# Kernel tuning notes

Hardware: AMD Instinct MI355X
Metric: run time of the kernel (lower is better)

## Reference

```python
import jax, jax.numpy as jnp
import numpy as np

N_NODES = 10000
N_EDGES = 320000
IN_DIM = 256
OUT_DIM = 256
LN_EPS = 1e-5


def setup_inputs() -> dict:
    key = jax.random.key(0)
    ks = jax.random.split(key, 4)
    x = jax.random.normal(ks[0], (N_NODES, IN_DIM), dtype=jnp.float32)
    edge_index = jax.random.randint(ks[1], (2, N_EDGES), 0, N_NODES, dtype=jnp.int64)
    # Linear weights stored input-major so y = x @ W + b
    W_msg = jax.random.normal(ks[2], (2 * IN_DIM, OUT_DIM), dtype=jnp.float32) / np.sqrt(2 * IN_DIM)
    b_msg = jnp.zeros((OUT_DIM,), dtype=jnp.float32)
    W_upd = jax.random.normal(ks[3], (IN_DIM + OUT_DIM, OUT_DIM), dtype=jnp.float32) / np.sqrt(IN_DIM + OUT_DIM)
    b_upd = jnp.zeros((OUT_DIM,), dtype=jnp.float32)
    gamma = jnp.ones((OUT_DIM,), dtype=jnp.float32)
    beta = jnp.zeros((OUT_DIM,), dtype=jnp.float32)
    return {"x": x, "edge_index": edge_index, "W_msg": W_msg, "b_msg": b_msg,
            "W_upd": W_upd, "b_upd": b_upd, "gamma": gamma, "beta": beta}


def reference(x, edge_index, W_msg, b_msg, W_upd, b_upd, gamma, beta):
    row, col = edge_index[0], edge_index[1]
    # gather -> concat -> linear -> relu   [E, out_dim]
    msg_in = jnp.concatenate([x[row], x[col]], axis=-1)
    messages = jax.nn.relu(msg_in @ W_msg + b_msg)
    # scatter-add aggregate over destination nodes  [N, out_dim]
    aggregated = jax.ops.segment_sum(messages, col, num_segments=x.shape[0])
    # update: concat -> linear -> relu -> layernorm
    h = jax.nn.relu(jnp.concatenate([x, aggregated], axis=-1) @ W_upd + b_upd)
    mu = jnp.mean(h, axis=-1, keepdims=True)
    var = jnp.mean(jnp.square(h - mu), axis=-1, keepdims=True)
    return (h - mu) * jax.lax.rsqrt(var + LN_EPS) * gamma + beta
```

## Files before the change

### kernel.cpp

```cpp
#include <hip/hip_runtime.h>
#include <hip/hip_bf16.h>
#include <stdint.h>

#define NNODES 10000
#define NEDGES 320000
#define DIM    256
#define KTOT   512
#define LN_EPS 1e-5f
#define BCAP   96

typedef __attribute__((ext_vector_type(4))) float f32x4;
typedef __attribute__((ext_vector_type(8))) short bf16x8;

__device__ __forceinline__ ushort f2bf(float f) {
    union { float f; uint32_t u; } v; v.f = f;
    uint32_t r = v.u + 0x7fffu + ((v.u >> 16) & 1u);
    return (ushort)(r >> 16);
}
__device__ __forceinline__ float bf2f(ushort u) {
    union { float f; uint32_t u; } v; v.u = ((uint32_t)u) << 16;
    return v.f;
}

__global__ __launch_bounds__(256)
void prep_all(const float* __restrict__ x, const float* __restrict__ Wm,
              const float* __restrict__ Wu, ushort* __restrict__ xb,
              ushort* __restrict__ Wcat, ushort* __restrict__ Wua,
              int4* __restrict__ cntz) {
    int tid = blockIdx.x * 256 + threadIdx.x;
    if (tid < 2560) cntz[tid] = (int4){0, 0, 0, 0};
    if (tid < 640000) {
        float4 v = reinterpret_cast<const float4*>(x)[tid];
        ushort4 o;
        o.x = f2bf(v.x); o.y = f2bf(v.y); o.z = f2bf(v.z); o.w = f2bf(v.w);
        reinterpret_cast<ushort4*>(xb)[tid] = o;
    } else {
        int t = tid - 640000;
        if (t < 131072) {
            int kk  = t >> 14;
            int rem = t & 16383;
            int g   = rem >> 9;
            int kg  = (rem >> 7) & 3;
            int ml  = (rem >> 3) & 15;
            int j   = rem & 7;
            int k = kk * 32 + kg * 8 + j;
            int n = g * 16 + ml;
            float v = (n < 256) ? Wm[k * DIM + n] : Wm[(k + 256) * DIM + (n - 256)];
            Wcat[t] = f2bf(v);
        } else {
            int rem = t - 131072;
            int kk  = rem >> 13;
            int nt  = (rem >> 9) & 15;
            int kg  = (rem >> 7) & 3;
            int ml  = (rem >> 3) & 15;
            int j   = rem & 7;
            int k = kk * 32 + kg * 8 + j;
            int n = nt * 16 + ml;
            Wua[rem] = f2bf(Wu[k * DIM + n]);
        }
    }
}

__global__ __launch_bounds__(512)
void scatter_uv(const int* __restrict__ eidx, int* __restrict__ cnt,
                int* __restrict__ srow, const ushort* __restrict__ xb,
                const ushort* __restrict__ Wcat, const float* __restrict__ bmsg,
                ushort* __restrict__ Ub, float* __restrict__ Vf) {
    if (blockIdx.x < 1250) {
        int e = blockIdx.x * 256 + (threadIdx.x & 255);
        if (threadIdx.x < 256) {
            int d = eidx[NEDGES + e];
            int p = atomicAdd(&cnt[d], 1);
            if (p < BCAP) srow[d * BCAP + p] = eidx[e];
        }
        return;
    }
    const int wave = threadIdx.x >> 6;
    const int lane = threadIdx.x & 63;
    const int ml = lane & 15, kg = lane >> 4;
    const int wr = wave >> 2, wc = wave & 3;
    const int nb = (blockIdx.x - 1250) * 64;

    uint arow[2];
#pragma unroll
    for (int t = 0; t < 2; ++t) {
        int n = nb + wr * 32 + t * 16 + ml;
        arow[t] = (uint)(n < NNODES ? n : NNODES - 1) * DIM;
    }

    f32x4 acc[2][8];
#pragma unroll
    for (int t = 0; t < 2; ++t)
#pragma unroll
        for (int nt = 0; nt < 8; ++nt) acc[t][nt] = (f32x4){0.f, 0.f, 0.f, 0.f};

#pragma unroll
    for (int kk = 0; kk < 8; ++kk) {
        bf16x8 a0 = *reinterpret_cast<const bf16x8*>(xb + arow[0] + kk * 32 + kg * 8);
        bf16x8 a1 = *reinterpret_cast<const bf16x8*>(xb + arow[1] + kk * 32 + kg * 8);
#pragma unroll
        for (int nt = 0; nt < 8; ++nt) {
            bf16x8 b = *reinterpret_cast<const bf16x8*>(Wcat + kk * 16384 + (wc * 8 + nt) * 512 + lane * 8);
            acc[0][nt] = __builtin_amdgcn_mfma_f32_16x16x32_bf16(a0, b, acc[0][nt], 0, 0, 0);
            acc[1][nt] = __builtin_amdgcn_mfma_f32_16x16x32_bf16(a1, b, acc[1][nt], 0, 0, 0);
        }
    }

    if (wc < 2) {
#pragma unroll
        for (int t = 0; t < 2; ++t)
#pragma unroll
            for (int nt = 0; nt < 8; ++nt) {
                const int col = wc * 128 + nt * 16 + ml;
#pragma unroll
                for (int i = 0; i < 4; ++i) {
                    int node = nb + wr * 32 + t * 16 + kg * 4 + i;
                    if (node < NNODES) Ub[(size_t)node * 256 + col] = f2bf(acc[t][nt][i]);
                }
            }
    } else {
#pragma unroll
        for (int t = 0; t < 2; ++t)
#pragma unroll
            for (int nt = 0; nt < 8; ++nt) {
                const int col = (wc - 2) * 128 + nt * 16 + ml;
                const float bb = bmsg[col];
#pragma unroll
                for (int i = 0; i < 4; ++i) {
                    int node = nb + wr * 32 + t * 16 + kg * 4 + i;
                    if (node < NNODES) Vf[(size_t)node * 256 + col] = acc[t][nt][i] + bb;
                }
            }
    }
}

__global__ __launch_bounds__(256)
void edge_combine(const ushort* __restrict__ Ub, const float* __restrict__ Vf,
                  const int* __restrict__ srow, const int* __restrict__ cnt,
                  ushort* __restrict__ aggb) {
    const int wave = threadIdx.x >> 6, lane = threadIdx.x & 63;
    const int nb = blockIdx.x * 8;
    const int el = lane >> 5;
    const int cl = lane & 31;
    const int c0 = cl * 8;

#pragma unroll
    for (int nn = 0; nn < 2; ++nn) {
        const int d = nb + wave * 2 + nn;
        int deg = cnt[d]; deg = deg < BCAP ? deg : BCAP;
        const int beg = d * BCAP;
        const float4 va = *reinterpret_cast<const float4*>(&Vf[(size_t)d * 256 + c0]);
        const float4 vb = *reinterpret_cast<const float4*>(&Vf[(size_t)d * 256 + c0 + 4]);
        float s[8];
#pragma unroll
        for (int j = 0; j < 8; ++j) s[j] = 0.f;

#define ACC8(U) do { \
        s[0] += fmaxf(bf2f((ushort)(U)[0]) + va.x, 0.f); \
        s[1] += fmaxf(bf2f((ushort)(U)[1]) + va.y, 0.f); \
        s[2] += fmaxf(bf2f((ushort)(U)[2]) + va.z, 0.f); \
        s[3] += fmaxf(bf2f((ushort)(U)[3]) + va.w, 0.f); \
        s[4] += fmaxf(bf2f((ushort)(U)[4]) + vb.x, 0.f); \
        s[5] += fmaxf(bf2f((ushort)(U)[5]) + vb.y, 0.f); \
        s[6] += fmaxf(bf2f((ushort)(U)[6]) + vb.z, 0.f); \
        s[7] += fmaxf(bf2f((ushort)(U)[7]) + vb.w, 0.f); } while (0)

        int i = el;
        for (; i + 6 < deg; i += 8) {
            int r0 = srow[beg + i],     r1 = srow[beg + i + 2];
            int r2 = srow[beg + i + 4], r3 = srow[beg + i + 6];
            bf16x8 u0 = *reinterpret_cast<const bf16x8*>(&Ub[(size_t)r0 * 256 + c0]);
            bf16x8 u1 = *reinterpret_cast<const bf16x8*>(&Ub[(size_t)r1 * 256 + c0]);
            bf16x8 u2 = *reinterpret_cast<const bf16x8*>(&Ub[(size_t)r2 * 256 + c0]);
            bf16x8 u3 = *reinterpret_cast<const bf16x8*>(&Ub[(size_t)r3 * 256 + c0]);
            ACC8(u0); ACC8(u1); ACC8(u2); ACC8(u3);
        }
        for (; i < deg; i += 2) {
            int r = srow[beg + i];
            bf16x8 u = *reinterpret_cast<const bf16x8*>(&Ub[(size_t)r * 256 + c0]);
            ACC8(u);
        }
#undef ACC8
#pragma unroll
        for (int j = 0; j < 8; ++j) s[j] += __shfl_xor(s[j], 32);
        if (el == 0) {
            union { bf16x8 v; ushort h[8]; } o;
#pragma unroll
            for (int j = 0; j < 8; ++j) o.h[j] = f2bf(s[j]);
            *reinterpret_cast<bf16x8*>(&aggb[(size_t)d * 256 + c0]) = o.v;
        }
    }
}

__global__ __launch_bounds__(512)
void node_ln(const ushort* __restrict__ xb, const ushort* __restrict__ aggb,
             const ushort* __restrict__ Wua, const float* __restrict__ bupd,
             const float* __restrict__ gamma, const float* __restrict__ beta,
             float* __restrict__ out) {
    __shared__ float pS[64][4][2];

    const int wave = threadIdx.x >> 6;
    const int lane = threadIdx.x & 63;
    const int ml = lane & 15, kg = lane >> 4;
    const int wr = wave >> 2, wc = wave & 3;
    const int nb = blockIdx.x * 64;

    uint arow[2];
#pragma unroll
    for (int t = 0; t < 2; ++t) {
        int n = nb + wr * 32 + t * 16 + ml;
        arow[t] = (uint)(n < NNODES ? n : NNODES - 1) * DIM;
    }

    f32x4 acc[2][4];
#pragma unroll
    for (int t = 0; t < 2; ++t)
#pragma unroll
        for (int nt = 0; nt < 4; ++nt) acc[t][nt] = (f32x4){0.f, 0.f, 0.f, 0.f};

#pragma unroll
    for (int kk = 0; kk < 8; ++kk) {
        bf16x8 a0 = *reinterpret_cast<const bf16x8*>(xb + arow[0] + kk * 32 + kg * 8);
        bf16x8 a1 = *reinterpret_cast<const bf16x8*>(xb + arow[1] + kk * 32 + kg * 8);
#pragma unroll
        for (int nt = 0; nt < 4; ++nt) {
            bf16x8 b = *reinterpret_cast<const bf16x8*>(Wua + kk * 8192 + (wc * 4 + nt) * 512 + lane * 8);
            acc[0][nt] = __builtin_amdgcn_mfma_f32_16x16x32_bf16(a0, b, acc[0][nt], 0, 0, 0);
            acc[1][nt] = __builtin_amdgcn_mfma_f32_16x16x32_bf16(a1, b, acc[1][nt], 0, 0, 0);
        }
    }
#pragma unroll
    for (int kk = 0; kk < 8; ++kk) {
        bf16x8 a0 = *reinterpret_cast<const bf16x8*>(aggb + arow[0] + kk * 32 + kg * 8);
        bf16x8 a1 = *reinterpret_cast<const bf16x8*>(aggb + arow[1] + kk * 32 + kg * 8);
#pragma unroll
        for (int nt = 0; nt < 4; ++nt) {
            bf16x8 b = *reinterpret_cast<const bf16x8*>(Wua + 65536 + kk * 8192 + (wc * 4 + nt) * 512 + lane * 8);
            acc[0][nt] = __builtin_amdgcn_mfma_f32_16x16x32_bf16(a0, b, acc[0][nt], 0, 0, 0);
            acc[1][nt] = __builtin_amdgcn_mfma_f32_16x16x32_bf16(a1, b, acc[1][nt], 0, 0, 0);
        }
    }

    float sum[2][4], ssq[2][4];
#pragma unroll
    for (int t = 0; t < 2; ++t)
#pragma unroll
        for (int i = 0; i < 4; ++i) { sum[t][i] = 0.f; ssq[t][i] = 0.f; }
#pragma unroll
    for (int t = 0; t < 2; ++t)
#pragma unroll
        for (int nt = 0; nt < 4; ++nt) {
            const float bb = bupd[wc * 64 + nt * 16 + ml];
#pragma unroll
            for (int i = 0; i < 4; ++i) {
                float v = acc[t][nt][i] + bb;
                v = v > 0.f ? v : 0.f;
                acc[t][nt][i] = v;
                sum[t][i] += v;
                ssq[t][i] += v * v;
            }
        }
#pragma unroll
    for (int m = 1; m < 16; m <<= 1) {
#pragma unroll
        for (int t = 0; t < 2; ++t)
#pragma unroll
            for (int i = 0; i < 4; ++i) {
                sum[t][i] += __shfl_xor(sum[t][i], m);
                ssq[t][i] += __shfl_xor(ssq[t][i], m);
            }
    }
    if (ml == 0) {
#pragma unroll
        for (int t = 0; t < 2; ++t)
#pragma unroll
            for (int i = 0; i < 4; ++i) {
                int nl = wr * 32 + t * 16 + kg * 4 + i;
                pS[nl][wc][0] = sum[t][i];
                pS[nl][wc][1] = ssq[t][i];
            }
    }
    __syncthreads();

    float mu[2][4], rs[2][4];
#pragma unroll
    for (int t = 0; t < 2; ++t)
#pragma unroll
        for (int i = 0; i < 4; ++i) {
            int nl = wr * 32 + t * 16 + kg * 4 + i;
            float S = pS[nl][0][0] + pS[nl][1][0] + pS[nl][2][0] + pS[nl][3][0];
            float Q = pS[nl][0][1] + pS[nl][1][1] + pS[nl][2][1] + pS[nl][3][1];
            float m = S * (1.f / 256.f);
            float var = Q * (1.f / 256.f) - m * m;
            mu[t][i] = m;
            rs[t][i] = rsqrtf(var + LN_EPS);
        }
#pragma unroll
    for (int t = 0; t < 2; ++t)
#pragma unroll
        for (int nt = 0; nt < 4; ++nt) {
            const int cc = wc * 64 + nt * 16 + ml;
            const float g = gamma[cc], be = beta[cc];
#pragma unroll
            for (int i = 0; i < 4; ++i) {
                const int node = nb + wr * 32 + t * 16 + kg * 4 + i;
                if (node < NNODES)
                    out[(size_t)node * DIM + cc] = (acc[t][nt][i] - mu[t][i]) * rs[t][i] * g + be;
            }
        }
}

extern "C" void kernel_launch(void* const* d_in, const int* in_sizes, int n_in,
                              void* d_out, int out_size, void* d_ws, size_t ws_size,
                              hipStream_t stream) {
    const float* x    = (const float*)d_in[0];
    const int*   eidx = (const int*)  d_in[1];
    const float* Wm   = (const float*)d_in[2];
    const float* bm   = (const float*)d_in[3];
    const float* Wu   = (const float*)d_in[4];
    const float* bu   = (const float*)d_in[5];
    const float* gam  = (const float*)d_in[6];
    const float* bet  = (const float*)d_in[7];
    float* out = (float*)d_out;

    char* ws = (char*)d_ws;
    ushort* xb     = (ushort*)(ws);
    ushort* Ub     = (ushort*)(ws +  5120000);
    float*  Vf     = (float*) (ws + 10240000);
    ushort* aggb   = (ushort*)(ws + 20480000);
    ushort* Wcat   = (ushort*)(ws + 25600000);
    ushort* Wua    = (ushort*)(ws + 25862144);
    int*    cnt    = (int*)   (ws + 26124288);
    int*    srow   = (int*)   (ws + 26165248);

    prep_all<<<3524, 256, 0, stream>>>(x, Wm, Wu, xb, Wcat, Wua, (int4*)cnt);
    scatter_uv<<<1407, 512, 0, stream>>>(eidx, cnt, srow, xb, Wcat, bm, Ub, Vf);
    edge_combine<<<1250, 256, 0, stream>>>(Ub, Vf, srow, cnt, aggb);
    node_ln<<<157, 512, 0, stream>>>(xb, aggb, Wua, bu, gam, bet, out);
}
```

Before: 87.41 us.

## Batch edge scatter per thread, shrink srow to ushort, retile node GEMM blocks

```diff
diff --git a/kernel.cpp b/kernel.cpp
--- a/kernel.cpp
+++ b/kernel.cpp
@@ -61,82 +61,75 @@
     }
 }
 
-__global__ __launch_bounds__(512)
+__global__ __launch_bounds__(256)
 void scatter_uv(const int* __restrict__ eidx, int* __restrict__ cnt,
-                int* __restrict__ srow, const ushort* __restrict__ xb,
+                ushort* __restrict__ srow, const ushort* __restrict__ xb,
                 const ushort* __restrict__ Wcat, const float* __restrict__ bmsg,
                 ushort* __restrict__ Ub, float* __restrict__ Vf) {
-    if (blockIdx.x < 1250) {
-        int e = blockIdx.x * 256 + (threadIdx.x & 255);
-        if (threadIdx.x < 256) {
-            int d = eidx[NEDGES + e];
-            int p = atomicAdd(&cnt[d], 1);
-            if (p < BCAP) srow[d * BCAP + p] = eidx[e];
-        }
+    if (blockIdx.x < 320) {
+        const int t = blockIdx.x * 256 + threadIdx.x;
+        int d[4], r[4];
+#pragma unroll
+        for (int j = 0; j < 3; ++j) {
+            int e = t + j * 81920;
+            d[j] = eidx[NEDGES + e];
+            r[j] = eidx[e];
+        }
+        const bool ok3 = t < (NEDGES - 3 * 81920);
+        if (ok3) { d[3] = eidx[NEDGES + t + 245760]; r[3] = eidx[t + 245760]; }
+        int p[4];
+#pragma unroll
+        for (int j = 0; j < 3; ++j) p[j] = atomicAdd(&cnt[d[j]], 1);
+        if (ok3) p[3] = atomicAdd(&cnt[d[3]], 1);
+#pragma unroll
+        for (int j = 0; j < 3; ++j)
+            if (p[j] < BCAP) srow[d[j] * BCAP + p[j]] = (ushort)r[j];
+        if (ok3 && p[3] < BCAP) srow[d[3] * BCAP + p[3]] = (ushort)r[3];
         return;
     }
-    const int wave = threadIdx.x >> 6;
+    const int wq   = threadIdx.x >> 6;
     const int lane = threadIdx.x & 63;
     const int ml = lane & 15, kg = lane >> 4;
-    const int wr = wave >> 2, wc = wave & 3;
-    const int nb = (blockIdx.x - 1250) * 64;
-
-    uint arow[2];
-#pragma unroll
-    for (int t = 0; t < 2; ++t) {
-        int n = nb + wr * 32 + t * 16 + ml;
-        arow[t] = (uint)(n < NNODES ? n : NNODES - 1) * DIM;
-    }
-
-    f32x4 acc[2][8];
-#pragma unroll
-    for (int t = 0; t < 2; ++t)
-#pragma unroll
-        for (int nt = 0; nt < 8; ++nt) acc[t][nt] = (f32x4){0.f, 0.f, 0.f, 0.f};
+    const int nb = (blockIdx.x - 320) * 16;
+    const uint arow = (uint)(nb + ml) * DIM;
+
+    f32x4 acc[8];
+#pragma unroll
+    for (int nt = 0; nt < 8; ++nt) acc[nt] = (f32x4){0.f, 0.f, 0.f, 0.f};
 
 #pragma unroll
     for (int kk = 0; kk < 8; ++kk) {
-        bf16x8 a0 = *reinterpret_cast<const bf16x8*>(xb + arow[0] + kk * 32 + kg * 8);
-        bf16x8 a1 = *reinterpret_cast<const bf16x8*>(xb + arow[1] + kk * 32 + kg * 8);
+        bf16x8 a = *reinterpret_cast<const bf16x8*>(xb + arow + kk * 32 + kg * 8);
 #pragma unroll
         for (int nt = 0; nt < 8; ++nt) {
-            bf16x8 b = *reinterpret_cast<const bf16x8*>(Wcat + kk * 16384 + (wc * 8 + nt) * 512 + lane * 8);
-            acc[0][nt] = __builtin_amdgcn_mfma_f32_16x16x32_bf16(a0, b, acc[0][nt], 0, 0, 0);
-            acc[1][nt] = __builtin_amdgcn_mfma_f32_16x16x32_bf16(a1, b, acc[1][nt], 0, 0, 0);
-        }
-    }
-
-    if (wc < 2) {
-#pragma unroll
-        for (int t = 0; t < 2; ++t)
-#pragma unroll
-            for (int nt = 0; nt < 8; ++nt) {
-                const int col = wc * 128 + nt * 16 + ml;
-#pragma unroll
-                for (int i = 0; i < 4; ++i) {
-                    int node = nb + wr * 32 + t * 16 + kg * 4 + i;
-                    if (node < NNODES) Ub[(size_t)node * 256 + col] = f2bf(acc[t][nt][i]);
-                }
-            }
+            bf16x8 b = *reinterpret_cast<const bf16x8*>(Wcat + kk * 16384 + (wq * 8 + nt) * 512 + lane * 8);
+            acc[nt] = __builtin_amdgcn_mfma_f32_16x16x32_bf16(a, b, acc[nt], 0, 0, 0);
+        }
+    }
+
+    if (wq < 2) {
+#pragma unroll
+        for (int nt = 0; nt < 8; ++nt) {
+            const int col = wq * 128 + nt * 16 + ml;
+#pragma unroll
+            for (int i = 0; i < 4; ++i)
+                Ub[(size_t)(nb + kg * 4 + i) * 256 + col] = f2bf(acc[nt][i]);
+        }
     } else {
 #pragma unroll
-        for (int t = 0; t < 2; ++t)
-#pragma unroll
-            for (int nt = 0; nt < 8; ++nt) {
-                const int col = (wc - 2) * 128 + nt * 16 + ml;
-                const float bb = bmsg[col];
-#pragma unroll
-                for (int i = 0; i < 4; ++i) {
-                    int node = nb + wr * 32 + t * 16 + kg * 4 + i;
-                    if (node < NNODES) Vf[(size_t)node * 256 + col] = acc[t][nt][i] + bb;
-                }
-            }
+        for (int nt = 0; nt < 8; ++nt) {
+            const int col = (wq - 2) * 128 + nt * 16 + ml;
+            const float bb = bmsg[col];
+#pragma unroll
+            for (int i = 0; i < 4; ++i)
+                Vf[(size_t)(nb + kg * 4 + i) * 256 + col] = acc[nt][i] + bb;
+        }
     }
 }
 
 __global__ __launch_bounds__(256)
 void edge_combine(const ushort* __restrict__ Ub, const float* __restrict__ Vf,
-                  const int* __restrict__ srow, const int* __restrict__ cnt,
+                  const ushort* __restrict__ srow, const int* __restrict__ cnt,
                   ushort* __restrict__ aggb) {
     const int wave = threadIdx.x >> 6, lane = threadIdx.x & 63;
     const int nb = blockIdx.x * 8;
@@ -331,10 +324,10 @@
     ushort* Wcat   = (ushort*)(ws + 25600000);
     ushort* Wua    = (ushort*)(ws + 25862144);
     int*    cnt    = (int*)   (ws + 26124288);
-    int*    srow   = (int*)   (ws + 26165248);
+    ushort* srow   = (ushort*)(ws + 26165248);
 
     prep_all<<<3524, 256, 0, stream>>>(x, Wm, Wu, xb, Wcat, Wua, (int4*)cnt);
-    scatter_uv<<<1407, 512, 0, stream>>>(eidx, cnt, srow, xb, Wcat, bm, Ub, Vf);
+    scatter_uv<<<945, 256, 0, stream>>>(eidx, cnt, srow, xb, Wcat, bm, Ub, Vf);
     edge_combine<<<1250, 256, 0, stream>>>(Ub, Vf, srow, cnt, aggb);
     node_ln<<<157, 512, 0, stream>>>(xb, aggb, Wua, bu, gam, bet, out);
 }
```

New measurement: 80.69 us (median of 3 runs). -7.7%, faster.
